# Kernel optimization log

Measured on AMD Instinct MI355X. Metric: run time of the kernel, lower is better.

Reference implementation:

```python
import jax, jax.numpy as jnp
import numpy as np

B, N, K = 8, 512, 16            # batches, proposals per batch, knn neighbors
C_POOL = 256                    # pooled feature dim (hardcoded 256 in source)
G_MLP = [128, 128]              # GLOBAL_INFORMATION.MLP_LAYERS
IN_DIM = C_POOL + G_MLP[-1]     # gnn_input_dim = 384
LAYERS = [512, 512, 512]


def _xavier(key, shape):
    fan_out, fan_in = shape
    lim = np.sqrt(6.0 / (fan_in + fan_out))
    return jax.random.uniform(key, shape, jnp.float32, -lim, lim)


def setup_inputs() -> dict:
    key = jax.random.key(0)
    ks = jax.random.split(key, 12)
    rois = jax.random.normal(ks[0], (B, N, 7), jnp.float32)
    rois = rois.at[:, :, :3].multiply(20.0)  # spread box centers spatially
    pooled_features = jax.random.normal(ks[1], (B, N, C_POOL), jnp.float32)

    # knn_graph per batch (loop=False): edges (neighbor j -> center i)
    coords = rois[:, :, :3]
    d2 = jnp.sum((coords[:, :, None, :] - coords[:, None, :, :]) ** 2, -1)  # [B,N,N]
    d2 = d2 + jnp.eye(N, dtype=jnp.float32) * 1e9                           # no self loops
    _, nbr = jax.lax.top_k(-d2, K)                                          # [B,N,K]
    offs = (jnp.arange(B) * N)[:, None, None]
    src = (nbr + offs).reshape(-1)
    dst = (jnp.broadcast_to(jnp.arange(N)[None, :, None], (B, N, K)) + offs).reshape(-1)
    edge_index = jnp.stack([src, dst]).astype(jnp.int32)                    # [2, B*N*K]

    # global-information MLP params: Linear(7,128), Linear(128,128)
    gW1 = _xavier(ks[2], (G_MLP[0], 7)); gb1 = jnp.zeros((G_MLP[0],), jnp.float32)
    gW2 = _xavier(ks[3], (G_MLP[1], G_MLP[0])); gb2 = jnp.zeros((G_MLP[1],), jnp.float32)

    # EdgeConv fc params: in = 2*in_dim of layer
    fcW1 = _xavier(ks[4], (LAYERS[0], 2 * IN_DIM)); fcb1 = jnp.zeros((LAYERS[0],), jnp.float32)
    fcW2 = _xavier(ks[5], (LAYERS[1], 2 * LAYERS[0])); fcb2 = jnp.zeros((LAYERS[1],), jnp.float32)
    fcW3 = _xavier(ks[6], (LAYERS[2], 2 * LAYERS[1])); fcb3 = jnp.zeros((LAYERS[2],), jnp.float32)

    return dict(rois=rois, pooled_features=pooled_features, edge_index=edge_index,
                gW1=gW1, gb1=gb1, gW2=gW2, gb2=gb2,
                fcW1=fcW1, fcb1=fcb1, fcW2=fcW2, fcb2=fcb2, fcW3=fcW3, fcb3=fcb3)


def reference(rois, pooled_features, edge_index,
              gW1, gb1, gW2, gb2,
              fcW1, fcb1, fcW2, fcb2, fcW3, fcb3):
    # global information MLP on proposal boxes
    g = jax.nn.relu(rois @ gW1.T + gb1)
    g = jax.nn.relu(g @ gW2.T + gb2)                      # [B,N,128]
    x = jnp.concatenate([pooled_features, g], -1).reshape(-1, IN_DIM)  # [B*N, 384]

    src, dst = edge_index[0], edge_index[1]
    n_nodes = B * N
    feats = [x]
    for W, b in ((fcW1, fcb1), (fcW2, fcb2), (fcW3, fcb3)):
        x_i = x[dst]                                      # target features [E,d]
        x_j = x[src]                                      # source features [E,d]
        msg = jax.nn.relu(jnp.concatenate([x_j - x_i, x_i], -1) @ W.T + b)  # [E,out]
        x = jax.ops.segment_max(msg, dst, num_segments=n_nodes)  # scatter-max aggr
        feats.append(x)
    return jnp.concatenate(feats, -1)                     # [B*N, 384+512*3]
```

## Files before the change

kernel.cpp:

```cpp
#include <hip/hip_runtime.h>
#include <hip/hip_bf16.h>

#define BN_NODES 4096
#define KNN 16
#define C_POOL 256
#define G_DIM 128
#define IN_DIM 384
#define L_DIM 512
#define OUT_STRIDE 1920

#define X0_OFF 0
#define X1_OFF 384
#define X2_OFF 896
#define X3_OFF 1408

typedef __attribute__((ext_vector_type(8))) __bf16 bf16x8;
typedef __attribute__((ext_vector_type(4))) float floatx4;

static __device__ __forceinline__ ushort f2bf(float v) {
  return __builtin_bit_cast(ushort, __float2bfloat16(v));
}
static __device__ __forceinline__ float bf2f(ushort u) {
  return __builtin_bit_cast(float, ((unsigned)u) << 16);
}
static __device__ __forceinline__ void gld_lds(const ushort* g, ushort* l) {
  __builtin_amdgcn_global_load_lds(
      (const __attribute__((address_space(1))) void*)g,
      (__attribute__((address_space(3))) void*)l, 16, 0, 0);
}

__global__ __launch_bounds__(256) void prep_kernel(
    const float* __restrict__ rois, const float* __restrict__ pooled,
    const float* __restrict__ gW1, const float* __restrict__ gb1,
    const float* __restrict__ gW2, const float* __restrict__ gb2,
    const float* __restrict__ W0, const float* __restrict__ W1,
    const float* __restrict__ W2, float* __restrict__ out,
    ushort* __restrict__ Xb0, ushort* __restrict__ Wb0,
    ushort* __restrict__ Wb1, ushort* __restrict__ Wb2) {
  const int t = threadIdx.x;
  if (blockIdx.x >= 512) {
    int wi = blockIdx.x - 512;
    const float* W;
    ushort* Wb;
    int K, base;
    if (wi < 384) {
      W = W0; Wb = Wb0; K = IN_DIM; base = wi;
    } else if (wi < 896) {
      W = W1; Wb = Wb1; K = L_DIM; base = wi - 384;
    } else {
      W = W2; Wb = Wb2; K = L_DIM; base = wi - 896;
    }
    int elem = base * 1024 + t * 4;
    int j = elem / K;
    int k = elem - j * K;
    const float* srcp = (j < 512) ? W + (size_t)j * (2 * K) + k
                                  : W + (size_t)(j - 512) * (2 * K) + K + k;
    ushort4 pk;
    pk.x = f2bf(srcp[0]);
    pk.y = f2bf(srcp[1]);
    pk.z = f2bf(srcp[2]);
    pk.w = f2bf(srcp[3]);
    *(ushort4*)(Wb + (size_t)j * K + k) = pk;
    return;
  }
  const int nb = blockIdx.x * 8;
  const int c = t & 127;
  const int nh = t >> 7;
  __shared__ float rs[8 * 7];
  __shared__ __align__(16) float h1[8][G_DIM];
  if (t < 56) rs[t] = rois[(size_t)nb * 7 + t];
  __syncthreads();
  {
    float w1[7];
#pragma unroll
    for (int i = 0; i < 7; i++) w1[i] = gW1[c * 7 + i];
    float b1 = gb1[c];
#pragma unroll
    for (int n = nh * 4; n < nh * 4 + 4; n++) {
      float a = b1;
#pragma unroll
      for (int i = 0; i < 7; i++) a += rs[n * 7 + i] * w1[i];
      h1[n][c] = fmaxf(a, 0.f);
    }
  }
  __syncthreads();
  float acc[4];
  {
    float b2 = gb2[c];
#pragma unroll
    for (int n = 0; n < 4; n++) acc[n] = b2;
    const float4* w4 = (const float4*)(gW2 + (size_t)c * G_DIM);
#pragma unroll 4
    for (int kc = 0; kc < G_DIM / 4; kc++) {
      float4 wv = w4[kc];
#pragma unroll
      for (int n = 0; n < 4; n++) {
        float4 hv = ((const float4*)h1[nh * 4 + n])[kc];
        acc[n] += wv.x * hv.x + wv.y * hv.y + wv.z * hv.z + wv.w * hv.w;
      }
    }
  }
#pragma unroll
  for (int n = 0; n < 4; n++) {
    int node = nb + nh * 4 + n;
    float g = fmaxf(acc[n], 0.f);
    const float* prow = pooled + (size_t)node * C_POOL;
    float p0 = prow[c], p1 = prow[G_DIM + c];
    float* orow = out + (size_t)node * OUT_STRIDE;
    orow[c] = p0;
    orow[G_DIM + c] = p1;
    orow[C_POOL + c] = g;
    ushort* xrow = Xb0 + (size_t)node * IN_DIM;
    xrow[c] = f2bf(p0);
    xrow[G_DIM + c] = f2bf(p1);
    xrow[C_POOL + c] = f2bf(g);
  }
}

__global__ __launch_bounds__(256) void layer_kernel(
    const ushort* __restrict__ Xin, int ldx, int K,
    const ushort* __restrict__ Wb, const int* __restrict__ src,
    const float* __restrict__ bias, float* __restrict__ out, int out_off,
    ushort* __restrict__ Xout, int write_x) {
  __shared__ ushort sA[512 * 64];
  __shared__ ushort sB[32 * 512];
  __shared__ ushort sPQ[512 * 32];
  const int stripe = blockIdx.x;
  const int b = blockIdx.y;
  const int tid = threadIdx.x;
  const int lane = tid & 63;
  const int w = tid >> 6;
  const int fr = lane & 15;
  const int kc = lane >> 4;

  const ushort* Ab = Xin + (size_t)(b * 512) * ldx;

  const int nbt = (K >> 5) * 2;
  for (int r = 0; r < nbt / 4; r++) {
    int tb = w + 4 * r;
    int kt = tb >> 1, ct = tb & 1;
    const ushort* g =
        Wb + (size_t)(ct * 512 + stripe * 16 + fr) * K + kt * 32 + kc * 8;
    gld_lds(g, &sB[tb * 512 + lane * 8]);
  }

  floatx4 acc[8][2];
#pragma unroll
  for (int i = 0; i < 8; i++)
#pragma unroll
    for (int j = 0; j < 2; j++) acc[i][j] = (floatx4){0.f, 0.f, 0.f, 0.f};

  for (int k0 = 0; k0 < K; k0 += 64) {
#pragma unroll
    for (int r = 0; r < 16; r++) {
      int ta = w + 4 * r;
      int rt = ta >> 1, ks = ta & 1;
      const ushort* g =
          Ab + (size_t)(rt * 16 + fr) * ldx + k0 + ks * 32 + kc * 8;
      gld_lds(g, &sA[ta * 512 + lane * 8]);
    }
    __syncthreads();
#pragma unroll
    for (int ks = 0; ks < 2; ks++) {
      int ktg = (k0 >> 5) + ks;
      bf16x8 bfv[2];
#pragma unroll
      for (int ct = 0; ct < 2; ct++)
        bfv[ct] = *(const bf16x8*)&sB[(ktg * 2 + ct) * 512 + lane * 8];
#pragma unroll
      for (int rl = 0; rl < 8; rl++) {
        bf16x8 av = *(const bf16x8*)&sA[((w * 8 + rl) * 2 + ks) * 512 + lane * 8];
#pragma unroll
        for (int ct = 0; ct < 2; ct++)
          acc[rl][ct] = __builtin_amdgcn_mfma_f32_16x16x32_bf16(av, bfv[ct],
                                                                acc[rl][ct], 0,
                                                                0, 0);
      }
    }
    __syncthreads();
  }

#pragma unroll
  for (int rl = 0; rl < 8; rl++)
#pragma unroll
    for (int ct = 0; ct < 2; ct++)
#pragma unroll
      for (int r = 0; r < 4; r++)
        sPQ[((w * 8 + rl) * 16 + kc * 4 + r) * 32 + ct * 16 + fr] =
            f2bf(acc[rl][ct][r]);
  __syncthreads();

  const int cq = tid & 3;
  const int slice = tid >> 2;
  const int c0 = stripe * 16;
  const float4 bb = *(const float4*)&bias[c0 + cq * 4];
#pragma unroll
  for (int i = 0; i < 8; i++) {
    int n = slice * 8 + i;
    const int* sp = src + (size_t)(b * 512 + n) * KNN;
    float mx = -1e30f, my = -1e30f, mz = -1e30f, mw = -1e30f;
#pragma unroll
    for (int k = 0; k < KNN; k++) {
      int sl = sp[k] - b * 512;
      ushort4 u = *(const ushort4*)&sPQ[sl * 32 + cq * 4];
      mx = fmaxf(mx, bf2f(u.x));
      my = fmaxf(my, bf2f(u.y));
      mz = fmaxf(mz, bf2f(u.z));
      mw = fmaxf(mw, bf2f(u.w));
    }
    ushort4 pu = *(const ushort4*)&sPQ[n * 32 + cq * 4];
    ushort4 qu = *(const ushort4*)&sPQ[n * 32 + 16 + cq * 4];
    float4 res;
    res.x = fmaxf(mx - bf2f(pu.x) + bf2f(qu.x) + bb.x, 0.f);
    res.y = fmaxf(my - bf2f(pu.y) + bf2f(qu.y) + bb.y, 0.f);
    res.z = fmaxf(mz - bf2f(pu.z) + bf2f(qu.z) + bb.z, 0.f);
    res.w = fmaxf(mw - bf2f(pu.w) + bf2f(qu.w) + bb.w, 0.f);
    size_t node = (size_t)(b * 512 + n);
    *(float4*)(out + node * OUT_STRIDE + out_off + c0 + cq * 4) = res;
    if (write_x) {
      ushort4 pk;
      pk.x = f2bf(res.x);
      pk.y = f2bf(res.y);
      pk.z = f2bf(res.z);
      pk.w = f2bf(res.w);
      *(ushort4*)(Xout + node * L_DIM + c0 + cq * 4) = pk;
    }
  }
}

extern "C" void kernel_launch(void* const* d_in, const int* in_sizes, int n_in,
                              void* d_out, int out_size, void* d_ws,
                              size_t ws_size, hipStream_t stream) {
  const float* rois = (const float*)d_in[0];
  const float* pooled = (const float*)d_in[1];
  const int* edge_index = (const int*)d_in[2];
  const float* gW1 = (const float*)d_in[3];
  const float* gb1 = (const float*)d_in[4];
  const float* gW2 = (const float*)d_in[5];
  const float* gb2 = (const float*)d_in[6];
  const float* fcW[3] = {(const float*)d_in[7], (const float*)d_in[9],
                         (const float*)d_in[11]};
  const float* fcb[3] = {(const float*)d_in[8], (const float*)d_in[10],
                         (const float*)d_in[12]};
  float* out = (float*)d_out;
  const int* src = edge_index;

  char* ws = (char*)d_ws;
  ushort* Xb0 = (ushort*)ws;
  ushort* Xb1 = (ushort*)(ws + (size_t)4 * 1024 * 1024);
  ushort* Xb2 = (ushort*)(ws + (size_t)8 * 1024 * 1024);
  ushort* Wb0 = (ushort*)(ws + (size_t)12 * 1024 * 1024);
  ushort* Wb1 = (ushort*)(ws + (size_t)13 * 1024 * 1024);
  ushort* Wb2 = (ushort*)(ws + (size_t)14 * 1024 * 1024);

  prep_kernel<<<1920, 256, 0, stream>>>(rois, pooled, gW1, gb1, gW2, gb2,
                                        fcW[0], fcW[1], fcW[2], out, Xb0, Wb0,
                                        Wb1, Wb2);
  layer_kernel<<<dim3(32, 8), 256, 0, stream>>>(Xb0, IN_DIM, IN_DIM, Wb0, src,
                                                fcb[0], out, X1_OFF, Xb1, 1);
  layer_kernel<<<dim3(32, 8), 256, 0, stream>>>(Xb1, L_DIM, L_DIM, Wb1, src,
                                                fcb[1], out, X2_OFF, Xb2, 1);
  layer_kernel<<<dim3(32, 8), 256, 0, stream>>>(Xb2, L_DIM, L_DIM, Wb2, src,
                                                fcb[2], out, X3_OFF, nullptr,
                                                0);
}
```

Measured before the change: 183.2 us.

## Double-buffer A tiles, widen layer blocks to 512 threads, node-per-thread aggregation

Reworks the per-layer kernel to use 512 threads per block with double-buffered A-tile loads. The next 256-row half-chunk is prefetched into LDS while MFMAs run on the current one, replacing the load-sync-compute-sync pattern. The max aggregation now assigns one node per thread, covering all 16 columns with vectorized neighbor index loads, and pads sPQ rows to 36 to reduce bank conflicts. LDS use rises to about 100KB per block, so occupancy is limited even though launch bounds request 2 blocks per CU.

```diff
diff --git a/kernel.cpp b/kernel.cpp
--- a/kernel.cpp
+++ b/kernel.cpp
@@ -9,7 +9,6 @@
 #define L_DIM 512
 #define OUT_STRIDE 1920
 
-#define X0_OFF 0
 #define X1_OFF 384
 #define X2_OFF 896
 #define X3_OFF 1408
@@ -117,15 +116,15 @@
   }
 }
 
-__global__ __launch_bounds__(256) void layer_kernel(
+__global__ __launch_bounds__(512, 2) void layer_kernel(
     const ushort* __restrict__ Xin, int ldx, int K,
     const ushort* __restrict__ Wb, const int* __restrict__ src,
     const float* __restrict__ bias, float* __restrict__ out, int out_off,
     ushort* __restrict__ Xout, int write_x) {
-  __shared__ ushort sA[512 * 64];
-  __shared__ ushort sB[32 * 512];
-  __shared__ ushort sPQ[512 * 32];
-  const int stripe = blockIdx.x;
+  __shared__ __align__(16) ushort sA[2][16384];
+  __shared__ __align__(16) ushort sB[16384];
+  __shared__ __align__(16) ushort sPQ[512 * 36];
+  const int s = blockIdx.x;
   const int b = blockIdx.y;
   const int tid = threadIdx.x;
   const int lane = tid & 63;
@@ -134,96 +133,135 @@
   const int kc = lane >> 4;
 
   const ushort* Ab = Xin + (size_t)(b * 512) * ldx;
-
-  const int nbt = (K >> 5) * 2;
-  for (int r = 0; r < nbt / 4; r++) {
-    int tb = w + 4 * r;
-    int kt = tb >> 1, ct = tb & 1;
-    const ushort* g =
-        Wb + (size_t)(ct * 512 + stripe * 16 + fr) * K + kt * 32 + kc * 8;
-    gld_lds(g, &sB[tb * 512 + lane * 8]);
-  }
-
-  floatx4 acc[8][2];
-#pragma unroll
-  for (int i = 0; i < 8; i++)
+  const int nk = K >> 6;
+  const int nc = nk * 2;
+
+  {
+    int nbt = (K >> 5) * 2;
+    for (int r = 0; r < nbt / 8; r++) {
+      int tb = w + 8 * r;
+      int kt = tb >> 1, ct = tb & 1;
+      const ushort* g =
+          Wb + (size_t)(ct * 512 + s * 16 + fr) * K + kt * 32 + kc * 8;
+      gld_lds(g, &sB[tb * 512 + lane * 8]);
+    }
+  }
+#pragma unroll
+  for (int r = 0; r < 4; r++) {
+    int ta = w * 4 + r;
+    int rt = ta >> 1, ks = ta & 1;
+    const ushort* g = Ab + (size_t)(rt * 16 + fr) * ldx + ks * 32 + kc * 8;
+    gld_lds(g, &sA[0][ta * 512 + lane * 8]);
+  }
+  __syncthreads();
+
+  floatx4 acc[4][2];
+#pragma unroll
+  for (int i = 0; i < 4; i++)
 #pragma unroll
     for (int j = 0; j < 2; j++) acc[i][j] = (floatx4){0.f, 0.f, 0.f, 0.f};
 
-  for (int k0 = 0; k0 < K; k0 += 64) {
-#pragma unroll
-    for (int r = 0; r < 16; r++) {
-      int ta = w + 4 * r;
-      int rt = ta >> 1, ks = ta & 1;
-      const ushort* g =
-          Ab + (size_t)(rt * 16 + fr) * ldx + k0 + ks * 32 + kc * 8;
-      gld_lds(g, &sA[ta * 512 + lane * 8]);
-    }
-    __syncthreads();
-#pragma unroll
-    for (int ks = 0; ks < 2; ks++) {
-      int ktg = (k0 >> 5) + ks;
-      bf16x8 bfv[2];
+  int c = 0;
+  for (int k0i = 0; k0i < nk; k0i++) {
+    bf16x8 bf[2][2];
+#pragma unroll
+    for (int ks = 0; ks < 2; ks++)
 #pragma unroll
       for (int ct = 0; ct < 2; ct++)
-        bfv[ct] = *(const bf16x8*)&sB[(ktg * 2 + ct) * 512 + lane * 8];
-#pragma unroll
-      for (int rl = 0; rl < 8; rl++) {
-        bf16x8 av = *(const bf16x8*)&sA[((w * 8 + rl) * 2 + ks) * 512 + lane * 8];
-#pragma unroll
-        for (int ct = 0; ct < 2; ct++)
-          acc[rl][ct] = __builtin_amdgcn_mfma_f32_16x16x32_bf16(av, bfv[ct],
-                                                                acc[rl][ct], 0,
-                                                                0, 0);
-      }
-    }
-    __syncthreads();
-  }
-
-#pragma unroll
-  for (int rl = 0; rl < 8; rl++)
-#pragma unroll
-    for (int ct = 0; ct < 2; ct++)
-#pragma unroll
-      for (int r = 0; r < 4; r++)
-        sPQ[((w * 8 + rl) * 16 + kc * 4 + r) * 32 + ct * 16 + fr] =
-            f2bf(acc[rl][ct][r]);
+        bf[ct][ks] =
+            *(const bf16x8*)&sB[((k0i * 2 + ks) * 2 + ct) * 512 + lane * 8];
+#pragma unroll
+    for (int rb = 0; rb < 2; rb++, c++) {
+      const ushort* cur = sA[c & 1];
+      if (c + 1 < nc) {
+        int k0n = (c + 1) >> 1, rbn = (c + 1) & 1;
+        ushort* nxt = sA[(c + 1) & 1];
+#pragma unroll
+        for (int r = 0; r < 4; r++) {
+          int ta = w * 4 + r;
+          int rt = ta >> 1, ks = ta & 1;
+          const ushort* g = Ab + (size_t)(rbn * 256 + rt * 16 + fr) * ldx +
+                            k0n * 64 + ks * 32 + kc * 8;
+          gld_lds(g, &nxt[ta * 512 + lane * 8]);
+        }
+      }
+#pragma unroll
+      for (int i = 0; i < 2; i++) {
+#pragma unroll
+        for (int ks = 0; ks < 2; ks++) {
+          bf16x8 av =
+              *(const bf16x8*)&cur[((2 * w + i) * 2 + ks) * 512 + lane * 8];
+#pragma unroll
+          for (int ct = 0; ct < 2; ct++)
+            acc[rb * 2 + i][ct] = __builtin_amdgcn_mfma_f32_16x16x32_bf16(
+                av, bf[ct][ks], acc[rb * 2 + i][ct], 0, 0, 0);
+        }
+      }
+      __syncthreads();
+    }
+  }
+
+#pragma unroll
+  for (int rb = 0; rb < 2; rb++)
+#pragma unroll
+    for (int i = 0; i < 2; i++)
+#pragma unroll
+      for (int ct = 0; ct < 2; ct++)
+#pragma unroll
+        for (int r = 0; r < 4; r++)
+          sPQ[(rb * 256 + (2 * w + i) * 16 + kc * 4 + r) * 36 + ct * 16 + fr] =
+              f2bf(acc[rb * 2 + i][ct][r]);
   __syncthreads();
 
-  const int cq = tid & 3;
-  const int slice = tid >> 2;
-  const int c0 = stripe * 16;
-  const float4 bb = *(const float4*)&bias[c0 + cq * 4];
-#pragma unroll
-  for (int i = 0; i < 8; i++) {
-    int n = slice * 8 + i;
+  {
+    const int n = tid;
     const int* sp = src + (size_t)(b * 512 + n) * KNN;
-    float mx = -1e30f, my = -1e30f, mz = -1e30f, mw = -1e30f;
+    int nbr[KNN];
+#pragma unroll
+    for (int k4 = 0; k4 < 4; k4++) {
+      int4 v = ((const int4*)sp)[k4];
+      nbr[k4 * 4 + 0] = v.x - b * 512;
+      nbr[k4 * 4 + 1] = v.y - b * 512;
+      nbr[k4 * 4 + 2] = v.z - b * 512;
+      nbr[k4 * 4 + 3] = v.w - b * 512;
+    }
+    float m[16];
+#pragma unroll
+    for (int c4 = 0; c4 < 16; c4++) m[c4] = -1e30f;
 #pragma unroll
     for (int k = 0; k < KNN; k++) {
-      int sl = sp[k] - b * 512;
-      ushort4 u = *(const ushort4*)&sPQ[sl * 32 + cq * 4];
-      mx = fmaxf(mx, bf2f(u.x));
-      my = fmaxf(my, bf2f(u.y));
-      mz = fmaxf(mz, bf2f(u.z));
-      mw = fmaxf(mw, bf2f(u.w));
-    }
-    ushort4 pu = *(const ushort4*)&sPQ[n * 32 + cq * 4];
-    ushort4 qu = *(const ushort4*)&sPQ[n * 32 + 16 + cq * 4];
-    float4 res;
-    res.x = fmaxf(mx - bf2f(pu.x) + bf2f(qu.x) + bb.x, 0.f);
-    res.y = fmaxf(my - bf2f(pu.y) + bf2f(qu.y) + bb.y, 0.f);
-    res.z = fmaxf(mz - bf2f(pu.z) + bf2f(qu.z) + bb.z, 0.f);
-    res.w = fmaxf(mw - bf2f(pu.w) + bf2f(qu.w) + bb.w, 0.f);
-    size_t node = (size_t)(b * 512 + n);
-    *(float4*)(out + node * OUT_STRIDE + out_off + c0 + cq * 4) = res;
-    if (write_x) {
-      ushort4 pk;
-      pk.x = f2bf(res.x);
-      pk.y = f2bf(res.y);
-      pk.z = f2bf(res.z);
-      pk.w = f2bf(res.w);
-      *(ushort4*)(Xout + node * L_DIM + c0 + cq * 4) = pk;
+      const ushort* prow = &sPQ[nbr[k] * 36];
+#pragma unroll
+      for (int c4 = 0; c4 < 4; c4++) {
+        ushort4 u = *(const ushort4*)(prow + c4 * 4);
+        m[c4 * 4 + 0] = fmaxf(m[c4 * 4 + 0], bf2f(u.x));
+        m[c4 * 4 + 1] = fmaxf(m[c4 * 4 + 1], bf2f(u.y));
+        m[c4 * 4 + 2] = fmaxf(m[c4 * 4 + 2], bf2f(u.z));
+        m[c4 * 4 + 3] = fmaxf(m[c4 * 4 + 3], bf2f(u.w));
+      }
+    }
+    const ushort* own = &sPQ[n * 36];
+    float* orow = out + (size_t)(b * 512 + n) * OUT_STRIDE + out_off + s * 16;
+    ushort* xrow = Xout + (size_t)(b * 512 + n) * L_DIM + s * 16;
+#pragma unroll
+    for (int c4 = 0; c4 < 4; c4++) {
+      ushort4 pu = *(const ushort4*)(own + c4 * 4);
+      ushort4 qu = *(const ushort4*)(own + 16 + c4 * 4);
+      float4 bb = *(const float4*)&bias[s * 16 + c4 * 4];
+      float4 res;
+      res.x = fmaxf(m[c4 * 4 + 0] - bf2f(pu.x) + bf2f(qu.x) + bb.x, 0.f);
+      res.y = fmaxf(m[c4 * 4 + 1] - bf2f(pu.y) + bf2f(qu.y) + bb.y, 0.f);
+      res.z = fmaxf(m[c4 * 4 + 2] - bf2f(pu.z) + bf2f(qu.z) + bb.z, 0.f);
+      res.w = fmaxf(m[c4 * 4 + 3] - bf2f(pu.w) + bf2f(qu.w) + bb.w, 0.f);
+      *(float4*)(orow + c4 * 4) = res;
+      if (write_x) {
+        ushort4 pk;
+        pk.x = f2bf(res.x);
+        pk.y = f2bf(res.y);
+        pk.z = f2bf(res.z);
+        pk.w = f2bf(res.w);
+        *(ushort4*)(xrow + c4 * 4) = pk;
+      }
     }
   }
 }
@@ -256,11 +294,10 @@
   prep_kernel<<<1920, 256, 0, stream>>>(rois, pooled, gW1, gb1, gW2, gb2,
                                         fcW[0], fcW[1], fcW[2], out, Xb0, Wb0,
                                         Wb1, Wb2);
-  layer_kernel<<<dim3(32, 8), 256, 0, stream>>>(Xb0, IN_DIM, IN_DIM, Wb0, src,
+  layer_kernel<<<dim3(32, 8), 512, 0, stream>>>(Xb0, IN_DIM, IN_DIM, Wb0, src,
                                                 fcb[0], out, X1_OFF, Xb1, 1);
-  layer_kernel<<<dim3(32, 8), 256, 0, stream>>>(Xb1, L_DIM, L_DIM, Wb1, src,
+  layer_kernel<<<dim3(32, 8), 512, 0, stream>>>(Xb1, L_DIM, L_DIM, Wb1, src,
                                                 fcb[1], out, X2_OFF, Xb2, 1);
-  layer_kernel<<<dim3(32, 8), 256, 0, stream>>>(Xb2, L_DIM, L_DIM, Wb2, src,
-                                                fcb[2], out, X3_OFF, nullptr,
-                                                0);
-}
+  layer_kernel<<<dim3(32, 8), 512, 0, stream>>>(Xb2, L_DIM, L_DIM, Wb2, src,
+                                                fcb[2], out, X3_OFF, Xb2, 0);
+}
```

New measurement: 186.2 us. Within noise of the previous version (+1.7%).

## Use 1024-thread blocks with direct global MFMA operand loads, dropping LDS staging

Applied to the files above, without the earlier changes.

The layer kernel moves from 256 to 1024 threads per block. Each of the 16 waves now computes a 32x32 tile whose A and B fragments are read straight from global memory into registers, replacing the global_load_lds staging through shared memory and the per-k-step barriers. The sPQ scratch row is padded to 36 elements to reduce LDS bank conflicts. The neighbour max aggregation is redistributed as one node-half per thread with vectorised index loads. This aims to raise wave parallelism and cut shared-memory traffic and barriers, at the cost of redundant global and L2 reads of A and B across waves.

```diff
diff --git a/kernel.cpp b/kernel.cpp
--- a/kernel.cpp
+++ b/kernel.cpp
@@ -9,7 +9,6 @@
 #define L_DIM 512
 #define OUT_STRIDE 1920
 
-#define X0_OFF 0
 #define X1_OFF 384
 #define X2_OFF 896
 #define X3_OFF 1408
@@ -22,11 +21,6 @@
 }
 static __device__ __forceinline__ float bf2f(ushort u) {
   return __builtin_bit_cast(float, ((unsigned)u) << 16);
-}
-static __device__ __forceinline__ void gld_lds(const ushort* g, ushort* l) {
-  __builtin_amdgcn_global_load_lds(
-      (const __attribute__((address_space(1))) void*)g,
-      (__attribute__((address_space(3))) void*)l, 16, 0, 0);
 }
 
 __global__ __launch_bounds__(256) void prep_kernel(
@@ -117,15 +111,13 @@
   }
 }
 
-__global__ __launch_bounds__(256) void layer_kernel(
+__global__ __launch_bounds__(1024) void layer_kernel(
     const ushort* __restrict__ Xin, int ldx, int K,
     const ushort* __restrict__ Wb, const int* __restrict__ src,
     const float* __restrict__ bias, float* __restrict__ out, int out_off,
     ushort* __restrict__ Xout, int write_x) {
-  __shared__ ushort sA[512 * 64];
-  __shared__ ushort sB[32 * 512];
-  __shared__ ushort sPQ[512 * 32];
-  const int stripe = blockIdx.x;
+  __shared__ __align__(16) ushort sPQ[512 * 36];
+  const int s = blockIdx.x;
   const int b = blockIdx.y;
   const int tid = threadIdx.x;
   const int lane = tid & 63;
@@ -133,97 +125,92 @@
   const int fr = lane & 15;
   const int kc = lane >> 4;
 
-  const ushort* Ab = Xin + (size_t)(b * 512) * ldx;
-
-  const int nbt = (K >> 5) * 2;
-  for (int r = 0; r < nbt / 4; r++) {
-    int tb = w + 4 * r;
-    int kt = tb >> 1, ct = tb & 1;
-    const ushort* g =
-        Wb + (size_t)(ct * 512 + stripe * 16 + fr) * K + kt * 32 + kc * 8;
-    gld_lds(g, &sB[tb * 512 + lane * 8]);
-  }
-
-  floatx4 acc[8][2];
-#pragma unroll
-  for (int i = 0; i < 8; i++)
+  const ushort* A0 = Xin + (size_t)(b * 512 + w * 32 + fr) * ldx + kc * 8;
+  const ushort* A1 = A0 + (size_t)16 * ldx;
+  const ushort* B0 = Wb + (size_t)(s * 16 + fr) * K + kc * 8;
+  const ushort* B1 = Wb + (size_t)(512 + s * 16 + fr) * K + kc * 8;
+
+  floatx4 acc[2][2];
+#pragma unroll
+  for (int i = 0; i < 2; i++)
 #pragma unroll
     for (int j = 0; j < 2; j++) acc[i][j] = (floatx4){0.f, 0.f, 0.f, 0.f};
 
-  for (int k0 = 0; k0 < K; k0 += 64) {
-#pragma unroll
-    for (int r = 0; r < 16; r++) {
-      int ta = w + 4 * r;
-      int rt = ta >> 1, ks = ta & 1;
-      const ushort* g =
-          Ab + (size_t)(rt * 16 + fr) * ldx + k0 + ks * 32 + kc * 8;
-      gld_lds(g, &sA[ta * 512 + lane * 8]);
-    }
-    __syncthreads();
-#pragma unroll
-    for (int ks = 0; ks < 2; ks++) {
-      int ktg = (k0 >> 5) + ks;
-      bf16x8 bfv[2];
-#pragma unroll
-      for (int ct = 0; ct < 2; ct++)
-        bfv[ct] = *(const bf16x8*)&sB[(ktg * 2 + ct) * 512 + lane * 8];
-#pragma unroll
-      for (int rl = 0; rl < 8; rl++) {
-        bf16x8 av = *(const bf16x8*)&sA[((w * 8 + rl) * 2 + ks) * 512 + lane * 8];
-#pragma unroll
-        for (int ct = 0; ct < 2; ct++)
-          acc[rl][ct] = __builtin_amdgcn_mfma_f32_16x16x32_bf16(av, bfv[ct],
-                                                                acc[rl][ct], 0,
-                                                                0, 0);
-      }
-    }
-    __syncthreads();
-  }
-
-#pragma unroll
-  for (int rl = 0; rl < 8; rl++)
+  const int nkt = K >> 5;
+#pragma unroll 4
+  for (int kt = 0; kt < nkt; kt++) {
+    bf16x8 a0 = *(const bf16x8*)(A0 + kt * 32);
+    bf16x8 a1 = *(const bf16x8*)(A1 + kt * 32);
+    bf16x8 b0 = *(const bf16x8*)(B0 + kt * 32);
+    bf16x8 b1 = *(const bf16x8*)(B1 + kt * 32);
+    acc[0][0] = __builtin_amdgcn_mfma_f32_16x16x32_bf16(a0, b0, acc[0][0], 0, 0, 0);
+    acc[0][1] = __builtin_amdgcn_mfma_f32_16x16x32_bf16(a0, b1, acc[0][1], 0, 0, 0);
+    acc[1][0] = __builtin_amdgcn_mfma_f32_16x16x32_bf16(a1, b0, acc[1][0], 0, 0, 0);
+    acc[1][1] = __builtin_amdgcn_mfma_f32_16x16x32_bf16(a1, b1, acc[1][1], 0, 0, 0);
+  }
+
+#pragma unroll
+  for (int i = 0; i < 2; i++)
 #pragma unroll
     for (int ct = 0; ct < 2; ct++)
 #pragma unroll
       for (int r = 0; r < 4; r++)
-        sPQ[((w * 8 + rl) * 16 + kc * 4 + r) * 32 + ct * 16 + fr] =
-            f2bf(acc[rl][ct][r]);
+        sPQ[(w * 32 + i * 16 + kc * 4 + r) * 36 + ct * 16 + fr] =
+            f2bf(acc[i][ct][r]);
   __syncthreads();
 
-  const int cq = tid & 3;
-  const int slice = tid >> 2;
-  const int c0 = stripe * 16;
-  const float4 bb = *(const float4*)&bias[c0 + cq * 4];
-#pragma unroll
-  for (int i = 0; i < 8; i++) {
-    int n = slice * 8 + i;
+  {
+    const int n = tid >> 1;
+    const int h = tid & 1;
     const int* sp = src + (size_t)(b * 512 + n) * KNN;
-    float mx = -1e30f, my = -1e30f, mz = -1e30f, mw = -1e30f;
+    int nbr[KNN];
+#pragma unroll
+    for (int k4 = 0; k4 < 4; k4++) {
+      int4 v = ((const int4*)sp)[k4];
+      nbr[k4 * 4 + 0] = v.x - b * 512;
+      nbr[k4 * 4 + 1] = v.y - b * 512;
+      nbr[k4 * 4 + 2] = v.z - b * 512;
+      nbr[k4 * 4 + 3] = v.w - b * 512;
+    }
+    float m[8];
+#pragma unroll
+    for (int c = 0; c < 8; c++) m[c] = -1e30f;
 #pragma unroll
     for (int k = 0; k < KNN; k++) {
-      int sl = sp[k] - b * 512;
-      ushort4 u = *(const ushort4*)&sPQ[sl * 32 + cq * 4];
-      mx = fmaxf(mx, bf2f(u.x));
-      my = fmaxf(my, bf2f(u.y));
-      mz = fmaxf(mz, bf2f(u.z));
-      mw = fmaxf(mw, bf2f(u.w));
-    }
-    ushort4 pu = *(const ushort4*)&sPQ[n * 32 + cq * 4];
-    ushort4 qu = *(const ushort4*)&sPQ[n * 32 + 16 + cq * 4];
-    float4 res;
-    res.x = fmaxf(mx - bf2f(pu.x) + bf2f(qu.x) + bb.x, 0.f);
-    res.y = fmaxf(my - bf2f(pu.y) + bf2f(qu.y) + bb.y, 0.f);
-    res.z = fmaxf(mz - bf2f(pu.z) + bf2f(qu.z) + bb.z, 0.f);
-    res.w = fmaxf(mw - bf2f(pu.w) + bf2f(qu.w) + bb.w, 0.f);
-    size_t node = (size_t)(b * 512 + n);
-    *(float4*)(out + node * OUT_STRIDE + out_off + c0 + cq * 4) = res;
+      const ushort* pr = &sPQ[nbr[k] * 36 + h * 8];
+      ushort4 u0 = *(const ushort4*)pr;
+      ushort4 u1 = *(const ushort4*)(pr + 4);
+      m[0] = fmaxf(m[0], bf2f(u0.x));
+      m[1] = fmaxf(m[1], bf2f(u0.y));
+      m[2] = fmaxf(m[2], bf2f(u0.z));
+      m[3] = fmaxf(m[3], bf2f(u0.w));
+      m[4] = fmaxf(m[4], bf2f(u1.x));
+      m[5] = fmaxf(m[5], bf2f(u1.y));
+      m[6] = fmaxf(m[6], bf2f(u1.z));
+      m[7] = fmaxf(m[7], bf2f(u1.w));
+    }
+    const ushort* own = &sPQ[n * 36 + h * 8];
+    float res[8];
+#pragma unroll
+    for (int c = 0; c < 8; c++) {
+      float p = bf2f(own[c]);
+      float q = bf2f(own[16 + c]);
+      float bb = bias[s * 16 + h * 8 + c];
+      res[c] = fmaxf(m[c] - p + q + bb, 0.f);
+    }
+    float* orow = out + (size_t)(b * 512 + n) * OUT_STRIDE + out_off + s * 16 +
+                  h * 8;
+    *(float4*)orow = (float4){res[0], res[1], res[2], res[3]};
+    *(float4*)(orow + 4) = (float4){res[4], res[5], res[6], res[7]};
     if (write_x) {
-      ushort4 pk;
-      pk.x = f2bf(res.x);
-      pk.y = f2bf(res.y);
-      pk.z = f2bf(res.z);
-      pk.w = f2bf(res.w);
-      *(ushort4*)(Xout + node * L_DIM + c0 + cq * 4) = pk;
+      ushort* xrow = Xout + (size_t)(b * 512 + n) * L_DIM + s * 16 + h * 8;
+      ushort4 p0, p1;
+      p0.x = f2bf(res[0]); p0.y = f2bf(res[1]);
+      p0.z = f2bf(res[2]); p0.w = f2bf(res[3]);
+      p1.x = f2bf(res[4]); p1.y = f2bf(res[5]);
+      p1.z = f2bf(res[6]); p1.w = f2bf(res[7]);
+      *(ushort4*)xrow = p0;
+      *(ushort4*)(xrow + 4) = p1;
     }
   }
 }
@@ -256,11 +243,10 @@
   prep_kernel<<<1920, 256, 0, stream>>>(rois, pooled, gW1, gb1, gW2, gb2,
                                         fcW[0], fcW[1], fcW[2], out, Xb0, Wb0,
                                         Wb1, Wb2);
-  layer_kernel<<<dim3(32, 8), 256, 0, stream>>>(Xb0, IN_DIM, IN_DIM, Wb0, src,
-                                                fcb[0], out, X1_OFF, Xb1, 1);
-  layer_kernel<<<dim3(32, 8), 256, 0, stream>>>(Xb1, L_DIM, L_DIM, Wb1, src,
-                                                fcb[1], out, X2_OFF, Xb2, 1);
-  layer_kernel<<<dim3(32, 8), 256, 0, stream>>>(Xb2, L_DIM, L_DIM, Wb2, src,
-                                                fcb[2], out, X3_OFF, nullptr,
-                                                0);
-}
+  layer_kernel<<<dim3(32, 8), 1024, 0, stream>>>(Xb0, IN_DIM, IN_DIM, Wb0, src,
+                                                 fcb[0], out, X1_OFF, Xb1, 1);
+  layer_kernel<<<dim3(32, 8), 1024, 0, stream>>>(Xb1, L_DIM, L_DIM, Wb1, src,
+                                                 fcb[1], out, X2_OFF, Xb2, 1);
+  layer_kernel<<<dim3(32, 8), 1024, 0, stream>>>(Xb2, L_DIM, L_DIM, Wb2, src,
+                                                 fcb[2], out, X3_OFF, Xb2, 0);
+}
```

After: 197.6 us. 1.08x slower.
